# Kernel optimization log

Hardware: AMD Instinct MI355X
Metric: run time of the kernel (lower is better)

## Reference

```python
import jax, jax.numpy as jnp
import numpy as np

EPS = 1e-06


def setup_inputs() -> dict:
    key = jax.random.key(0)
    k1, k2 = jax.random.split(key)
    N, M, D = 8192, 8192, 512
    first_vector = jax.random.normal(k1, (N, D), dtype=jnp.float32)
    second_vector = jax.random.normal(k2, (M, D), dtype=jnp.float32)
    return {"first_vector": first_vector, "second_vector": second_vector, "normalize": 1}


def reference(first_vector, second_vector, normalize):
    # Pairwise dot products: [N, M]. Mathematically identical to the
    # broadcast multiply + sum over D in the torch module, but as a GEMM.
    sim = jnp.einsum('nd,md->nm', first_vector, second_vector)
    if normalize:
        # Note: module divides by sqrt(|a| * |b|) + eps (geometric mean of
        # norms, not the product) -- reproduce exactly.
        n1 = jnp.linalg.norm(first_vector, axis=1)[:, None]   # [N, 1]
        n2 = jnp.linalg.norm(second_vector, axis=1)[None, :]  # [1, M]
        sim = sim / (jnp.sqrt(n1 * n2) + EPS)
    return sim
```

## Files before the change

### kernel.cpp

```cpp
#include <hip/hip_runtime.h>
#include <hip/hip_bf16.h>
#include <math.h>

#define EPS 1e-6f

constexpr int D  = 512;
constexpr int BM = 128;
constexpr int BN = 128;
constexpr int BK = 32;

typedef __attribute__((ext_vector_type(8))) short  short8;
typedef __attribute__((ext_vector_type(4))) float  floatx4;

__global__ __launch_bounds__(256) void prep_kernel(
    const float* __restrict__ src, __hip_bfloat16* __restrict__ dst,
    float* __restrict__ isn) {
  const int row = blockIdx.x;
  const int t   = threadIdx.x;
  const float2 v = ((const float2*)(src + (size_t)row * D))[t];
  if (dst != nullptr) {
    __hip_bfloat16* drow = dst + (size_t)row * D;
    drow[2 * t]     = __float2bfloat16(v.x);
    drow[2 * t + 1] = __float2bfloat16(v.y);
  }
  float ss = v.x * v.x + v.y * v.y;
  #pragma unroll
  for (int o = 32; o > 0; o >>= 1) ss += __shfl_down(ss, o);
  __shared__ float red[4];
  if ((t & 63) == 0) red[t >> 6] = ss;
  __syncthreads();
  if (t == 0) {
    const float tot = red[0] + red[1] + red[2] + red[3];
    const float n1  = sqrtf(tot);
    isn[row] = 1.0f / sqrtf(n1);
  }
}

__global__ __launch_bounds__(256) void gemm_bt_kernel(
    const __hip_bfloat16* __restrict__ A, const __hip_bfloat16* __restrict__ B,
    const float* __restrict__ ia, const float* __restrict__ ib,
    const int* __restrict__ nrmflag, float* __restrict__ C,
    int N, int M) {
  __shared__ __align__(16) __hip_bfloat16 sA[BM * BK];
  __shared__ __align__(16) __hip_bfloat16 sB[BN * BK];

  const int t    = threadIdx.x;
  const int w    = t >> 6;
  const int lane = t & 63;
  const int wm   = w & 1;
  const int wn   = w >> 1;

  const size_t rowA0 = (size_t)blockIdx.x * BM;
  const size_t rowB0 = (size_t)blockIdx.y * BN;

  floatx4 acc[4][4];
  #pragma unroll
  for (int i = 0; i < 4; ++i)
    #pragma unroll
    for (int j = 0; j < 4; ++j) acc[i][j] = (floatx4){0.f, 0.f, 0.f, 0.f};

  const int ldRow = lane >> 2;
  const int ldCol = (lane & 3) * 8;
  const int fr = lane & 15;
  const int fq = (lane >> 4) * 8;

  const __hip_bfloat16* gA0 = A + (rowA0 + (size_t)ldRow) * D + ldCol;
  const __hip_bfloat16* gB0 = B + (rowB0 + (size_t)ldRow) * D + ldCol;

  for (int k0 = 0; k0 < D; k0 += BK) {
    #pragma unroll
    for (int j = 0; j < 2; ++j) {
      const int c = w * 2 + j;
      __builtin_amdgcn_global_load_lds(
          (const __attribute__((address_space(1))) void*)(gA0 + (size_t)(c * 16) * D + k0),
          (__attribute__((address_space(3))) void*)(sA + c * 512), 16, 0, 0);
      __builtin_amdgcn_global_load_lds(
          (const __attribute__((address_space(1))) void*)(gB0 + (size_t)(c * 16) * D + k0),
          (__attribute__((address_space(3))) void*)(sB + c * 512), 16, 0, 0);
    }
    __syncthreads();

    short8 af[4], bf[4];
    #pragma unroll
    for (int i = 0; i < 4; ++i) {
      af[i] = *(const short8*)(sA + (wm * 64 + i * 16 + fr) * BK + fq);
      bf[i] = *(const short8*)(sB + (wn * 64 + i * 16 + fr) * BK + fq);
    }
    #pragma unroll
    for (int i = 0; i < 4; ++i)
      #pragma unroll
      for (int j = 0; j < 4; ++j)
        acc[i][j] = __builtin_amdgcn_mfma_f32_16x16x32_bf16(af[i], bf[j], acc[i][j], 0, 0, 0);
    __syncthreads();
  }

  const int nrm = *nrmflag;
  const int cq  = lane >> 4;
  const int cc  = lane & 15;

  float ibv[4];
  #pragma unroll
  for (int j = 0; j < 4; ++j) ibv[j] = ib[rowB0 + wn * 64 + j * 16 + cc];

  #pragma unroll
  for (int i = 0; i < 4; ++i) {
    #pragma unroll
    for (int r = 0; r < 4; ++r) {
      const size_t row = rowA0 + wm * 64 + i * 16 + cq * 4 + r;
      const float iav  = ia[row];
      float* crow = C + row * (size_t)M + rowB0 + wn * 64 + cc;
      #pragma unroll
      for (int j = 0; j < 4; ++j) {
        float v = acc[i][j][r];
        if (nrm) v *= iav * ibv[j];
        crow[j * 16] = v;
      }
    }
  }
}

__global__ __launch_bounds__(256) void fb_gemm(
    const float* __restrict__ A, const float* __restrict__ B,
    const float* __restrict__ ia, const float* __restrict__ ib,
    const int* __restrict__ nrmflag, float* __restrict__ C, int N, int M) {
  __shared__ float sA[32][33];
  __shared__ float sB[32][33];
  const int tx = threadIdx.x & 31;
  const int ty = threadIdx.x >> 5;
  const size_t row0 = (size_t)blockIdx.y * 32;
  const size_t col0 = (size_t)blockIdx.x * 32;
  float acc[4] = {0.f, 0.f, 0.f, 0.f};
  for (int k0 = 0; k0 < D; k0 += 32) {
    #pragma unroll
    for (int r = 0; r < 4; ++r) {
      sA[ty + 8 * r][tx] = A[(row0 + ty + 8 * r) * D + k0 + tx];
      sB[ty + 8 * r][tx] = B[(col0 + ty + 8 * r) * D + k0 + tx];
    }
    __syncthreads();
    #pragma unroll 8
    for (int kk = 0; kk < 32; ++kk) {
      const float bv = sB[tx][kk];
      #pragma unroll
      for (int r = 0; r < 4; ++r) acc[r] += sA[ty + 8 * r][kk] * bv;
    }
    __syncthreads();
  }
  const int nrm  = *nrmflag;
  const float iv = ib[col0 + tx];
  #pragma unroll
  for (int r = 0; r < 4; ++r) {
    const size_t row = row0 + ty + 8 * r;
    float v = acc[r];
    if (nrm) {
      const float denom = 1.0f / (ia[row] * iv) + EPS;
      v /= denom;
    }
    C[row * (size_t)M + col0 + tx] = v;
  }
}

extern "C" void kernel_launch(void* const* d_in, const int* in_sizes, int n_in,
                              void* d_out, int out_size, void* d_ws, size_t ws_size,
                              hipStream_t stream) {
  const float* A   = (const float*)d_in[0];
  const float* B   = (const float*)d_in[1];
  const int*   nrm = (const int*)d_in[2];
  float*       C   = (float*)d_out;
  const int N = in_sizes[0] / D;
  const int M = in_sizes[1] / D;

  float* iaN = (float*)d_ws;
  float* ibN = iaN + N;
  __hip_bfloat16* Abf = (__hip_bfloat16*)(ibN + M);
  __hip_bfloat16* Bbf = Abf + (size_t)N * D;

  const size_t need = (size_t)(N + M) * sizeof(float)
                    + (size_t)(N + M) * D * sizeof(__hip_bfloat16);
  const bool fast = (ws_size >= need) && (N % BM == 0) && (M % BN == 0);

  prep_kernel<<<N, 256, 0, stream>>>(A, fast ? Abf : nullptr, iaN);
  prep_kernel<<<M, 256, 0, stream>>>(B, fast ? Bbf : nullptr, ibN);

  if (fast) {
    gemm_bt_kernel<<<dim3(N / BM, M / BN), 256, 0, stream>>>(Abf, Bbf, iaN, ibN, nrm, C, N, M);
  } else {
    fb_gemm<<<dim3(M / 32, N / 32), 256, 0, stream>>>(A, B, iaN, ibN, nrm, C, N, M);
  }
}
```

Baseline: 356.2 us.

## Widen GEMM K-step to 64, vectorize prep kernel, streamline epilogue scaling

```diff
diff --git a/kernel.cpp b/kernel.cpp
--- a/kernel.cpp
+++ b/kernel.cpp
@@ -7,31 +7,42 @@
 constexpr int D  = 512;
 constexpr int BM = 128;
 constexpr int BN = 128;
-constexpr int BK = 32;
 
 typedef __attribute__((ext_vector_type(8))) short  short8;
 typedef __attribute__((ext_vector_type(4))) float  floatx4;
 
+__device__ inline unsigned short f2bf(float f) {
+  union { __hip_bfloat16 h; unsigned short u; } cvt;
+  cvt.h = __float2bfloat16(f);
+  return cvt.u;
+}
+
 __global__ __launch_bounds__(256) void prep_kernel(
     const float* __restrict__ src, __hip_bfloat16* __restrict__ dst,
-    float* __restrict__ isn) {
-  const int row = blockIdx.x;
-  const int t   = threadIdx.x;
-  const float2 v = ((const float2*)(src + (size_t)row * D))[t];
+    float* __restrict__ isn, int nrows) {
+  const int lane = threadIdx.x & 63;
+  const int row  = blockIdx.x * 4 + (threadIdx.x >> 6);
+  if (row >= nrows) return;
+
+  const float4* p4 = (const float4*)(src + (size_t)row * D);
+  const float4 v1 = p4[lane];
+  const float4 v2 = p4[lane + 64];
+
   if (dst != nullptr) {
-    __hip_bfloat16* drow = dst + (size_t)row * D;
-    drow[2 * t]     = __float2bfloat16(v.x);
-    drow[2 * t + 1] = __float2bfloat16(v.y);
-  }
-  float ss = v.x * v.x + v.y * v.y;
+    ushort4 u1, u2;
+    u1.x = f2bf(v1.x); u1.y = f2bf(v1.y); u1.z = f2bf(v1.z); u1.w = f2bf(v1.w);
+    u2.x = f2bf(v2.x); u2.y = f2bf(v2.y); u2.z = f2bf(v2.z); u2.w = f2bf(v2.w);
+    ushort4* drow = (ushort4*)(dst + (size_t)row * D);
+    drow[lane]      = u1;
+    drow[lane + 64] = u2;
+  }
+
+  float ss = v1.x * v1.x + v1.y * v1.y + v1.z * v1.z + v1.w * v1.w
+           + v2.x * v2.x + v2.y * v2.y + v2.z * v2.z + v2.w * v2.w;
   #pragma unroll
   for (int o = 32; o > 0; o >>= 1) ss += __shfl_down(ss, o);
-  __shared__ float red[4];
-  if ((t & 63) == 0) red[t >> 6] = ss;
-  __syncthreads();
-  if (t == 0) {
-    const float tot = red[0] + red[1] + red[2] + red[3];
-    const float n1  = sqrtf(tot);
+  if (lane == 0) {
+    const float n1 = sqrtf(ss);
     isn[row] = 1.0f / sqrtf(n1);
   }
 }
@@ -41,8 +52,8 @@
     const float* __restrict__ ia, const float* __restrict__ ib,
     const int* __restrict__ nrmflag, float* __restrict__ C,
     int N, int M) {
-  __shared__ __align__(16) __hip_bfloat16 sA[BM * BK];
-  __shared__ __align__(16) __hip_bfloat16 sB[BN * BK];
+  __shared__ __align__(16) __hip_bfloat16 sA[2][BM * 32];
+  __shared__ __align__(16) __hip_bfloat16 sB[2][BN * 32];
 
   const int t    = threadIdx.x;
   const int w    = t >> 6;
@@ -67,30 +78,37 @@
   const __hip_bfloat16* gA0 = A + (rowA0 + (size_t)ldRow) * D + ldCol;
   const __hip_bfloat16* gB0 = B + (rowB0 + (size_t)ldRow) * D + ldCol;
 
-  for (int k0 = 0; k0 < D; k0 += BK) {
-    #pragma unroll
-    for (int j = 0; j < 2; ++j) {
-      const int c = w * 2 + j;
-      __builtin_amdgcn_global_load_lds(
-          (const __attribute__((address_space(1))) void*)(gA0 + (size_t)(c * 16) * D + k0),
-          (__attribute__((address_space(3))) void*)(sA + c * 512), 16, 0, 0);
-      __builtin_amdgcn_global_load_lds(
-          (const __attribute__((address_space(1))) void*)(gB0 + (size_t)(c * 16) * D + k0),
-          (__attribute__((address_space(3))) void*)(sB + c * 512), 16, 0, 0);
-    }
-    __syncthreads();
-
-    short8 af[4], bf[4];
-    #pragma unroll
-    for (int i = 0; i < 4; ++i) {
-      af[i] = *(const short8*)(sA + (wm * 64 + i * 16 + fr) * BK + fq);
-      bf[i] = *(const short8*)(sB + (wn * 64 + i * 16 + fr) * BK + fq);
-    }
-    #pragma unroll
-    for (int i = 0; i < 4; ++i)
-      #pragma unroll
-      for (int j = 0; j < 4; ++j)
-        acc[i][j] = __builtin_amdgcn_mfma_f32_16x16x32_bf16(af[i], bf[j], acc[i][j], 0, 0, 0);
+  for (int k0 = 0; k0 < D; k0 += 64) {
+    #pragma unroll
+    for (int h = 0; h < 2; ++h) {
+      const int kc = k0 + h * 32;
+      #pragma unroll
+      for (int j = 0; j < 2; ++j) {
+        const int c = w * 2 + j;
+        __builtin_amdgcn_global_load_lds(
+            (const __attribute__((address_space(1))) void*)(gA0 + (size_t)(c * 16) * D + kc),
+            (__attribute__((address_space(3))) void*)(&sA[h][c * 512]), 16, 0, 0);
+        __builtin_amdgcn_global_load_lds(
+            (const __attribute__((address_space(1))) void*)(gB0 + (size_t)(c * 16) * D + kc),
+            (__attribute__((address_space(3))) void*)(&sB[h][c * 512]), 16, 0, 0);
+      }
+    }
+    __syncthreads();
+
+    #pragma unroll
+    for (int h = 0; h < 2; ++h) {
+      short8 af[4], bf[4];
+      #pragma unroll
+      for (int i = 0; i < 4; ++i) {
+        af[i] = *(const short8*)(&sA[h][(wm * 64 + i * 16 + fr) * 32 + fq]);
+        bf[i] = *(const short8*)(&sB[h][(wn * 64 + i * 16 + fr) * 32 + fq]);
+      }
+      #pragma unroll
+      for (int i = 0; i < 4; ++i)
+        #pragma unroll
+        for (int j = 0; j < 4; ++j)
+          acc[i][j] = __builtin_amdgcn_mfma_f32_16x16x32_bf16(af[i], bf[j], acc[i][j], 0, 0, 0);
+    }
     __syncthreads();
   }
 
@@ -100,21 +118,21 @@
 
   float ibv[4];
   #pragma unroll
-  for (int j = 0; j < 4; ++j) ibv[j] = ib[rowB0 + wn * 64 + j * 16 + cc];
+  for (int j = 0; j < 4; ++j)
+    ibv[j] = nrm ? ib[rowB0 + wn * 64 + j * 16 + cc] : 1.0f;
 
   #pragma unroll
   for (int i = 0; i < 4; ++i) {
+    const size_t rbase = rowA0 + wm * 64 + i * 16 + cq * 4;
+    float4 iav4 = nrm ? *(const float4*)(ia + rbase) : (float4){1.f, 1.f, 1.f, 1.f};
+    const float iavr[4] = {iav4.x, iav4.y, iav4.z, iav4.w};
     #pragma unroll
     for (int r = 0; r < 4; ++r) {
-      const size_t row = rowA0 + wm * 64 + i * 16 + cq * 4 + r;
-      const float iav  = ia[row];
+      const size_t row = rbase + r;
       float* crow = C + row * (size_t)M + rowB0 + wn * 64 + cc;
       #pragma unroll
-      for (int j = 0; j < 4; ++j) {
-        float v = acc[i][j][r];
-        if (nrm) v *= iav * ibv[j];
-        crow[j * 16] = v;
-      }
+      for (int j = 0; j < 4; ++j)
+        crow[j * 16] = acc[i][j][r] * iavr[r] * ibv[j];
     }
   }
 }
@@ -178,8 +196,8 @@
                     + (size_t)(N + M) * D * sizeof(__hip_bfloat16);
   const bool fast = (ws_size >= need) && (N % BM == 0) && (M % BN == 0);
 
-  prep_kernel<<<N, 256, 0, stream>>>(A, fast ? Abf : nullptr, iaN);
-  prep_kernel<<<M, 256, 0, stream>>>(B, fast ? Bbf : nullptr, ibN);
+  prep_kernel<<<(N + 3) / 4, 256, 0, stream>>>(A, fast ? Abf : nullptr, iaN, N);
+  prep_kernel<<<(M + 3) / 4, 256, 0, stream>>>(B, fast ? Bbf : nullptr, ibN, M);
 
   if (fast) {
     gemm_bt_kernel<<<dim3(N / BM, M / BN), 256, 0, stream>>>(Abf, Bbf, iaN, ibN, nrm, C, N, M);
```

Measured after the change: 346.4 us. 1.03x faster.
